# Optimization experiments

Hardware: AMD Instinct MI355X
Metric: run time of the kernel (lower is better)

The kernel has to match this reference:

```python
import jax, jax.numpy as jnp
import numpy as np

TAU, LBDA, THETA = 0.25, 0.15, 0.3
N_WARPS, N_ITERS = 5, 5
EPS = 1e-12  # GRAD_IS_ZERO


def centered_gradient(x):
    # centered [-0.5,0,0.5] stencil with one-sided boundaries (matches conv+boundary-fix)
    dx = jnp.concatenate([0.5 * (x[..., 1:2] - x[..., 0:1]),
                          0.5 * (x[..., 2:] - x[..., :-2]),
                          0.5 * (x[..., -1:] - x[..., -2:-1])], axis=-1)
    dy = jnp.concatenate([0.5 * (x[:, :, 1:2] - x[:, :, 0:1]),
                          0.5 * (x[:, :, 2:] - x[:, :, :-2]),
                          0.5 * (x[:, :, -1:] - x[:, :, -2:-1])], axis=2)
    return dx, dy


def forward_gradient(x):
    # [-1,1] forward difference, zero at last col/row (conv 'same' + zeroed last slice)
    dx = jnp.concatenate([x[..., 1:] - x[..., :-1], jnp.zeros_like(x[..., :1])], axis=-1)
    dy = jnp.concatenate([x[:, :, 1:] - x[:, :, :-1], jnp.zeros_like(x[:, :, :1])], axis=2)
    return dx, dy


def forward_divergence(px, py):
    # backward difference with zero left/top boundary; last entry = -p[-2]
    dx = jnp.concatenate([px[..., :1], px[..., 1:-1] - px[..., :-2], -px[..., -2:-1]], axis=-1)
    dy = jnp.concatenate([py[:, :, :1], py[:, :, 1:-1] - py[:, :, :-2], -py[:, :, -2:-1]], axis=2)
    return dx + dy


def warp_image(im, u, v):
    # bilinear warp by pixel flow (u,v); grid math mirrors the STN spatial_transformer:
    # normalized identity grid in [-1,1] plus flow*2/size, mapped back via (g+1)*size/2,
    # with indices clipped to the image (border behavior).
    B, C, H, W = im.shape
    dt = im.dtype
    gx = jnp.linspace(-1.0, 1.0, W, dtype=dt)[None, None, None, :]
    gy = jnp.linspace(-1.0, 1.0, H, dtype=dt)[None, None, :, None]
    x = (gx + u * (2.0 / W) + 1.0) * (W / 2.0)
    y = (gy + v * (2.0 / H) + 1.0) * (H / 2.0)
    x0 = jnp.floor(x).astype(jnp.int32)
    y0 = jnp.floor(y).astype(jnp.int32)
    x0i = jnp.clip(x0, 0, W - 1); x1i = jnp.clip(x0 + 1, 0, W - 1)
    y0i = jnp.clip(y0, 0, H - 1); y1i = jnp.clip(y0 + 1, 0, H - 1)
    x0f = x0i.astype(dt); x1f = x1i.astype(dt)
    y0f = y0i.astype(dt); y1f = y1i.astype(dt)
    flat = im.reshape(B, H * W)

    def gather(yi, xi):
        idx = (yi * W + xi).reshape(B, H * W)
        return jnp.take_along_axis(flat, idx, axis=1).reshape(B, C, H, W)

    Ia = gather(y0i, x0i); Ib = gather(y1i, x0i)
    Ic = gather(y0i, x1i); Id = gather(y1i, x1i)
    wa = (x1f - x) * (y1f - y); wb = (x1f - x) * (y - y0f)
    wc = (x - x0f) * (y1f - y); wd = (x - x0f) * (y - y0f)
    return wa * Ia + wb * Ib + wc * Ic + wd * Id


def tv_l1_scale(x1, x2, u1, u2):
    l_t = LBDA * THETA
    taut = TAU / THETA
    d2x, d2y = centered_gradient(x2)
    z = jnp.zeros_like(x1)
    p11, p12, p21, p22 = z, z, z, z
    rho = z
    for _ in range(N_WARPS):
        x2w = warp_image(x2, u1, u2)
        dxw = warp_image(d2x, u1, u2)
        dyw = warp_image(d2y, u1, u2)
        grad = dxw * dxw + dyw * dyw + EPS
        rho_c = x2w - dxw * u1 - dyw * u2 - x1
        for _ in range(N_ITERS):
            rho = rho_c + dxw * u1 + dyw * u2 + EPS
            m1 = rho < -l_t * grad
            m2 = rho > l_t * grad
            m3 = (~m1) & (~m2) & (grad > EPS)
            s = jnp.where(m1, l_t, jnp.where(m2, -l_t, jnp.where(m3, -rho / grad, 0.0)))
            v1 = s * dxw + u1
            v2 = s * dyw + u2
            u1 = v1 + THETA * forward_divergence(p11, p12)
            u2 = v2 + THETA * forward_divergence(p21, p22)
            u1x, u1y = forward_gradient(u1)
            u2x, u2y = forward_gradient(u2)
            n1 = 1.0 + taut * jnp.sqrt(u1x * u1x + u1y * u1y + EPS)
            n2 = 1.0 + taut * jnp.sqrt(u2x * u2x + u2y * u2y + EPS)
            p11 = (p11 + taut * u1x) / n1
            p12 = (p12 + taut * u1y) / n1
            p21 = (p21 + taut * u2x) / n2
            p22 = (p22 + taut * u2y) / n2
    return u1, u2, rho


def setup_inputs() -> dict:
    key = jax.random.key(0)
    k1, k2 = jax.random.split(key)
    B, H, W = 8, 480, 480
    x1 = jax.random.uniform(k1, (B, 1, H, W), dtype=jnp.float32)
    x2 = jax.random.uniform(k2, (B, 1, H, W), dtype=jnp.float32)
    u1 = jnp.zeros((B, 1, H, W), dtype=jnp.float32)
    u2 = jnp.zeros((B, 1, H, W), dtype=jnp.float32)
    return {"x1": x1, "x2": x2, "u1": u1, "u2": u2}


def reference(x1, x2, u1, u2):
    return tv_l1_scale(x1, x2, u1, u2)
```

## Files before the change

kernel.cpp:

```cpp
#include <hip/hip_runtime.h>

#pragma clang fp contract(off)


constexpr int B = 8, H = 480, W = 480;
constexpr int HW = H * W;
constexpr int N = B * HW;

constexpr float THETA = (float)0.3;
constexpr float L_T  = (float)(0.15 * 0.3);
constexpr float TAUT = (float)(0.25 / 0.3);
constexpr float EPSF = (float)1e-12;

#define RW 50
#define RH 40
#define HALO 5
#define TW (RW - 2*HALO)
#define TH (RH - 2*HALO)
#define NTX 12
#define NTY 16
#define TPB 512
#define NPX 4
#define RPX (RW*RH)

template <int LASTWARP>
__global__ __launch_bounds__(TPB, 4) void k_fused(
    const float* __restrict__ x1, const float* __restrict__ x2,
    const float* __restrict__ u1In, const float* __restrict__ u2In,
    const float* __restrict__ pIn,
    float* __restrict__ u1Out, float* __restrict__ u2Out,
    float* __restrict__ pOut,
    float* __restrict__ rhoOut)
{
  __shared__ float2 su[RH][RW];
  __shared__ float2 spA[RH][RW];
  __shared__ float2 spB[RH][RW];

  int blk = blockIdx.x;
  int bx = blk % NTX;
  int by = (blk / NTX) % NTY;
  int b  = blk / (NTX * NTY);
  int ox = bx * TW - HALO;
  int oy = by * TH - HALO;

  int tid = threadIdx.x;

  const float* __restrict__ im = x2 + b * HW;
  const int base = b * HW;

  float cdx[NPX], cdy[NPX], crc[NPX];

#pragma unroll
  for (int k = 0; k < NPX; ++k) {
    int idx = tid + k * TPB;
    if (idx < RPX) {
      int ly = idx / RW, lx = idx - ly * RW;
      int px = ox + lx, py = oy + ly;
      bool valid = (px >= 0 && px < W && py >= 0 && py < H);
      if (valid) {
        int gi = base + py * W + px;
        float u = u1In[gi], v = u2In[gi];
        const float step = 2.0f / 479.0f;
        float gx = -1.0f + (float)px * step;
        float gy = -1.0f + (float)py * step;
        float X = ((gx + u * (float)(2.0 / 480.0)) + 1.0f) * 240.0f;
        float Y = ((gy + v * (float)(2.0 / 480.0)) + 1.0f) * 240.0f;
        float fX = floorf(X), fY = floorf(Y);
        int ix = (int)fX, iy = (int)fY;
        int x0i = min(max(ix, 0), W - 1);
        int x1i = min(max(ix + 1, 0), W - 1);
        int y0i = min(max(iy, 0), H - 1);
        int y1i = min(max(iy + 1, 0), H - 1);
        float x0f = (float)x0i, x1f = (float)x1i;
        float y0f = (float)y0i, y1f = (float)y1i;
        float wa = (x1f - X) * (y1f - Y);
        float wb = (x1f - X) * (Y - y0f);
        float wc = (X - x0f) * (y1f - Y);
        float wd = (X - x0f) * (Y - y0f);
        auto at = [&](int yy, int xx) -> float { return im[yy * W + xx]; };
        auto dxc = [&](int yy, int xx) -> float {
          int xm = max(xx - 1, 0), xp = min(xx + 1, W - 1);
          return 0.5f * (at(yy, xp) - at(yy, xm));
        };
        auto dyc = [&](int yy, int xx) -> float {
          int ym = max(yy - 1, 0), yp = min(yy + 1, H - 1);
          return 0.5f * (at(yp, xx) - at(ym, xx));
        };
        float x2w = ((wa * at(y0i, x0i) + wb * at(y1i, x0i)) + wc * at(y0i, x1i)) + wd * at(y1i, x1i);
        float dxw = ((wa * dxc(y0i, x0i) + wb * dxc(y1i, x0i)) + wc * dxc(y0i, x1i)) + wd * dxc(y1i, x1i);
        float dyw = ((wa * dyc(y0i, x0i) + wb * dyc(y1i, x0i)) + wc * dyc(y0i, x1i)) + wd * dyc(y1i, x1i);
        cdx[k] = dxw; cdy[k] = dyw;
        crc[k] = ((x2w - dxw * u) - dyw * v) - x1[gi];
        float q11, q12, q21, q22;
        if (pIn) {
          q11 = pIn[0 * N + gi]; q12 = pIn[1 * N + gi];
          q21 = pIn[2 * N + gi]; q22 = pIn[3 * N + gi];
        } else { q11 = 0.f; q12 = 0.f; q21 = 0.f; q22 = 0.f; }
        su[ly][lx]  = make_float2(u, v);
        spA[ly][lx] = make_float2(q11, q21);
        spB[ly][lx] = make_float2(q12, q22);
      }
    }
  }
  __syncthreads();

  for (int t = 1; t <= 5; ++t) {
    int ulox = ox + t; if (ulox < 0) ulox = 0;
    int uloy = oy + t; if (uloy < 0) uloy = 0;
    int uhix = (ox + RW >= W) ? W : (ox + RW + 1 - t);
    int uhiy = (oy + RH >= H) ? H : (oy + RH + 1 - t);

#pragma unroll
    for (int k = 0; k < NPX; ++k) {
      int idx = tid + k * TPB;
      if (idx < RPX) {
        int ly = idx / RW, lx = idx - ly * RW;
        int px = ox + lx, py = oy + ly;
        if (px >= ulox && px < uhix && py >= uloy && py < uhiy) {
          float2 uo  = su[ly][lx];
          float2 pAo = spA[ly][lx];
          float2 pBo = spB[ly][lx];
          float2 pl = spA[ly][lx - 1];
          float2 pu = spB[ly - 1][lx];
          float dx = cdx[k], dy = cdy[k];
          float u = uo.x, v = uo.y;
          float rho = ((crc[k] + dx * u) + dy * v) + EPSF;
          float grad = (dx * dx + dy * dy) + EPSF;
          float lt_g = L_T * grad;
          float s;
          if (rho < -lt_g)      s = L_T;
          else if (rho > lt_g)  s = -L_T;
          else if (grad > EPSF) s = (-rho) / grad;
          else                  s = 0.f;
          float v1 = s * dx + u;
          float v2 = s * dy + v;
          float dvx1, dvy1, dvx2, dvy2;
          if (px == 0)          dvx1 = pAo.x;
          else if (px == W - 1) dvx1 = -pl.x;
          else                  dvx1 = pAo.x - pl.x;
          if (py == 0)          dvy1 = pBo.x;
          else if (py == H - 1) dvy1 = -pu.x;
          else                  dvy1 = pBo.x - pu.x;
          if (px == 0)          dvx2 = pAo.y;
          else if (px == W - 1) dvx2 = -pl.y;
          else                  dvx2 = pAo.y - pl.y;
          if (py == 0)          dvy2 = pBo.y;
          else if (py == H - 1) dvy2 = -pu.y;
          else                  dvy2 = pBo.y - pu.y;
          float nu1 = v1 + THETA * (dvx1 + dvy1);
          float nu2 = v2 + THETA * (dvx2 + dvy2);
          su[ly][lx] = make_float2(nu1, nu2);
          if (LASTWARP && t == 5) {
            int tx0 = bx * TW, ty0 = by * TH;
            if (px >= tx0 && px < tx0 + TW && py >= ty0 && py < ty0 + TH)
              rhoOut[base + py * W + px] = rho;
          }
        }
      }
    }
    __syncthreads();

    if (!(LASTWARP && t == 5)) {
      int phix = (ox + RW >= W) ? W : (ox + RW - t);
      int phiy = (oy + RH >= H) ? H : (oy + RH - t);
#pragma unroll
      for (int k = 0; k < NPX; ++k) {
        int idx = tid + k * TPB;
        if (idx < RPX) {
          int ly = idx / RW, lx = idx - ly * RW;
          int px = ox + lx, py = oy + ly;
          if (px >= ulox && px < phix && py >= uloy && py < phiy) {
            float2 uo = su[ly][lx];
            float2 uR = su[ly][lx + 1];
            float2 uD = su[ly + 1][lx];
            float2 pAo = spA[ly][lx];
            float2 pBo = spB[ly][lx];
            float u1c = uo.x, u2c = uo.y;
            float u1x = (px < W - 1) ? uR.x - u1c : 0.f;
            float u1y = (py < H - 1) ? uD.x - u1c : 0.f;
            float u2x = (px < W - 1) ? uR.y - u2c : 0.f;
            float u2y = (py < H - 1) ? uD.y - u2c : 0.f;
            float n1 = 1.0f + TAUT * sqrtf((u1x * u1x + u1y * u1y) + EPSF);
            float n2 = 1.0f + TAUT * sqrtf((u2x * u2x + u2y * u2y) + EPSF);
            float np11 = (pAo.x + TAUT * u1x) / n1;
            float np12 = (pBo.x + TAUT * u1y) / n1;
            float np21 = (pAo.y + TAUT * u2x) / n2;
            float np22 = (pBo.y + TAUT * u2y) / n2;
            spA[ly][lx] = make_float2(np11, np21);
            spB[ly][lx] = make_float2(np12, np22);
          }
        }
      }
    }
    __syncthreads();
  }

  int tx0 = bx * TW, ty0 = by * TH;
#pragma unroll
  for (int k = 0; k < NPX; ++k) {
    int idx = tid + k * TPB;
    if (idx < RPX) {
      int ly = idx / RW, lx = idx - ly * RW;
      int px = ox + lx, py = oy + ly;
      if (px >= tx0 && px < tx0 + TW && py >= ty0 && py < ty0 + TH) {
        int gi = base + py * W + px;
        float2 uo = su[ly][lx];
        u1Out[gi] = uo.x;
        u2Out[gi] = uo.y;
        if (!LASTWARP) {
          float2 pAo = spA[ly][lx];
          float2 pBo = spB[ly][lx];
          pOut[0 * N + gi] = pAo.x;
          pOut[1 * N + gi] = pBo.x;
          pOut[2 * N + gi] = pAo.y;
          pOut[3 * N + gi] = pBo.y;
        }
      }
    }
  }
}

extern "C" void kernel_launch(void* const* d_in, const int* in_sizes, int n_in,
                              void* d_out, int out_size, void* d_ws, size_t ws_size,
                              hipStream_t stream) {
  const float* x1 = (const float*)d_in[0];
  const float* x2 = (const float*)d_in[1];
  const float* u1_in = (const float*)d_in[2];
  const float* u2_in = (const float*)d_in[3];

  float* u1o  = (float*)d_out;
  float* u2o  = u1o + (size_t)N;
  float* rhoo = u1o + (size_t)2 * N;

  float* ws  = (float*)d_ws;
  float* uA1 = ws;
  float* uA2 = ws + (size_t)N;
  float* pA  = ws + (size_t)2 * N;
  float* uB1 = ws + (size_t)6 * N;
  float* uB2 = ws + (size_t)7 * N;
  float* pB  = ws + (size_t)8 * N;

  dim3 grd(NTX * NTY * B), blk(TPB);
  k_fused<0><<<grd, blk, 0, stream>>>(x1, x2, u1_in, u2_in, nullptr, uA1, uA2, pA, rhoo);
  k_fused<0><<<grd, blk, 0, stream>>>(x1, x2, uA1, uA2, pA, uB1, uB2, pB, rhoo);
  k_fused<0><<<grd, blk, 0, stream>>>(x1, x2, uB1, uB2, pB, uA1, uA2, pA, rhoo);
  k_fused<0><<<grd, blk, 0, stream>>>(x1, x2, uA1, uA2, pA, uB1, uB2, pB, rhoo);
  k_fused<1><<<grd, blk, 0, stream>>>(x1, x2, uB1, uB2, pB, u1o, u2o, pA, rhoo);
}
```

Before: 354.5 us.

## Interleave intermediate u/p state and specialize interior tiles without boundary checks

Intermediate flow and dual variables between warp launches are now stored interleaved, as float2 for u and float4 for p, so each pixel reads and writes state with one vector access instead of several strided scalar ones. Each block is dispatched to an interior or boundary template, and the interior version drops the image-edge clamps and divergence/gradient boundary branches. Local pixel coordinates are precomputed once per thread rather than recomputed with divisions every phase. The cost is roughly doubled code size from the two template instantiations, which may raise register pressure.

Result: slower. 365.9 us (+3.2%).

```diff
diff --git a/kernel.cpp b/kernel.cpp
--- a/kernel.cpp
+++ b/kernel.cpp
@@ -15,51 +15,53 @@
 #define RW 50
 #define RH 40
 #define HALO 5
-#define TW (RW - 2*HALO)
-#define TH (RH - 2*HALO)
+#define TW 40
+#define TH 30
 #define NTX 12
 #define NTY 16
 #define TPB 512
 #define NPX 4
 #define RPX (RW*RH)
 
-template <int LASTWARP>
-__global__ __launch_bounds__(TPB, 4) void k_fused(
+template <int WARPK, bool INTERIOR>
+__device__ __forceinline__ void run_body(
     const float* __restrict__ x1, const float* __restrict__ x2,
     const float* __restrict__ u1In, const float* __restrict__ u2In,
-    const float* __restrict__ pIn,
+    const float2* __restrict__ uIn, const float4* __restrict__ pIn,
     float* __restrict__ u1Out, float* __restrict__ u2Out,
-    float* __restrict__ pOut,
-    float* __restrict__ rhoOut)
+    float2* __restrict__ uOut, float4* __restrict__ pOut,
+    float* __restrict__ rhoOut,
+    int bx, int by, int b,
+    float2* __restrict__ su, float2* __restrict__ spA,
+    float2* __restrict__ spB)
 {
-  __shared__ float2 su[RH][RW];
-  __shared__ float2 spA[RH][RW];
-  __shared__ float2 spB[RH][RW];
-
-  int blk = blockIdx.x;
-  int bx = blk % NTX;
-  int by = (blk / NTX) % NTY;
-  int b  = blk / (NTX * NTY);
-  int ox = bx * TW - HALO;
-  int oy = by * TH - HALO;
-
-  int tid = threadIdx.x;
-
-  const float* __restrict__ im = x2 + b * HW;
+  const int ox = bx * TW - HALO;
+  const int oy = by * TH - HALO;
+  const int tid = threadIdx.x;
   const int base = b * HW;
+  const float* __restrict__ im = x2 + base;
 
   float cdx[NPX], cdy[NPX], crc[NPX];
+  int lxA[NPX], lyA[NPX];
+#pragma unroll
+  for (int k = 0; k < NPX; ++k) {
+    int idx = tid + k * TPB;
+    lyA[k] = idx / RW;
+    lxA[k] = idx - lyA[k] * RW;
+  }
 
 #pragma unroll
   for (int k = 0; k < NPX; ++k) {
     int idx = tid + k * TPB;
     if (idx < RPX) {
-      int ly = idx / RW, lx = idx - ly * RW;
+      int lx = lxA[k], ly = lyA[k];
       int px = ox + lx, py = oy + ly;
-      bool valid = (px >= 0 && px < W && py >= 0 && py < H);
+      bool valid = INTERIOR ? true : (px >= 0 && px < W && py >= 0 && py < H);
       if (valid) {
         int gi = base + py * W + px;
-        float u = u1In[gi], v = u2In[gi];
+        float u, v;
+        if (WARPK == 0) { u = u1In[gi]; v = u2In[gi]; }
+        else            { float2 uv = uIn[gi]; u = uv.x; v = uv.y; }
         const float step = 2.0f / 479.0f;
         float gx = -1.0f + (float)px * step;
         float gy = -1.0f + (float)py * step;
@@ -91,37 +93,41 @@
         float dyw = ((wa * dyc(y0i, x0i) + wb * dyc(y1i, x0i)) + wc * dyc(y0i, x1i)) + wd * dyc(y1i, x1i);
         cdx[k] = dxw; cdy[k] = dyw;
         crc[k] = ((x2w - dxw * u) - dyw * v) - x1[gi];
-        float q11, q12, q21, q22;
-        if (pIn) {
-          q11 = pIn[0 * N + gi]; q12 = pIn[1 * N + gi];
-          q21 = pIn[2 * N + gi]; q22 = pIn[3 * N + gi];
-        } else { q11 = 0.f; q12 = 0.f; q21 = 0.f; q22 = 0.f; }
-        su[ly][lx]  = make_float2(u, v);
-        spA[ly][lx] = make_float2(q11, q21);
-        spB[ly][lx] = make_float2(q12, q22);
+        float4 q;
+        if (WARPK == 0) q = make_float4(0.f, 0.f, 0.f, 0.f);
+        else            q = pIn[gi];
+        su[idx]  = make_float2(u, v);
+        spA[idx] = make_float2(q.x, q.z);
+        spB[idx] = make_float2(q.y, q.w);
       }
     }
   }
   __syncthreads();
 
   for (int t = 1; t <= 5; ++t) {
-    int ulox = ox + t; if (ulox < 0) ulox = 0;
-    int uloy = oy + t; if (uloy < 0) uloy = 0;
-    int uhix = (ox + RW >= W) ? W : (ox + RW + 1 - t);
-    int uhiy = (oy + RH >= H) ? H : (oy + RH + 1 - t);
+    int ulox, uloy, uhix, uhiy;
+    if (INTERIOR) {
+      ulox = ox + t; uloy = oy + t;
+      uhix = ox + RW + 1 - t; uhiy = oy + RH + 1 - t;
+    } else {
+      ulox = ox + t; if (ulox < 0) ulox = 0;
+      uloy = oy + t; if (uloy < 0) uloy = 0;
+      uhix = (ox + RW >= W) ? W : (ox + RW + 1 - t);
+      uhiy = (oy + RH >= H) ? H : (oy + RH + 1 - t);
+    }
 
 #pragma unroll
     for (int k = 0; k < NPX; ++k) {
       int idx = tid + k * TPB;
       if (idx < RPX) {
-        int ly = idx / RW, lx = idx - ly * RW;
+        int lx = lxA[k], ly = lyA[k];
         int px = ox + lx, py = oy + ly;
         if (px >= ulox && px < uhix && py >= uloy && py < uhiy) {
-          float2 uo  = su[ly][lx];
-          float2 pAo = spA[ly][lx];
-          float2 pBo = spB[ly][lx];
-          float2 pl = spA[ly][lx - 1];
-          float2 pu = spB[ly - 1][lx];
+          float2 uo  = su[idx];
+          float2 pAo = spA[idx];
+          float2 pBo = spB[idx];
+          float2 pl = spA[idx - 1];
+          float2 pu = spB[idx - RW];
           float dx = cdx[k], dy = cdy[k];
           float u = uo.x, v = uo.y;
           float rho = ((crc[k] + dx * u) + dy * v) + EPSF;
@@ -135,24 +141,30 @@
           float v1 = s * dx + u;
           float v2 = s * dy + v;
           float dvx1, dvy1, dvx2, dvy2;
-          if (px == 0)          dvx1 = pAo.x;
-          else if (px == W - 1) dvx1 = -pl.x;
-          else                  dvx1 = pAo.x - pl.x;
-          if (py == 0)          dvy1 = pBo.x;
-          else if (py == H - 1) dvy1 = -pu.x;
-          else                  dvy1 = pBo.x - pu.x;
-          if (px == 0)          dvx2 = pAo.y;
-          else if (px == W - 1) dvx2 = -pl.y;
-          else                  dvx2 = pAo.y - pl.y;
-          if (py == 0)          dvy2 = pBo.y;
-          else if (py == H - 1) dvy2 = -pu.y;
-          else                  dvy2 = pBo.y - pu.y;
+          if (INTERIOR) {
+            dvx1 = pAo.x - pl.x;
+            dvy1 = pBo.x - pu.x;
+            dvx2 = pAo.y - pl.y;
+            dvy2 = pBo.y - pu.y;
+          } else {
+            if (px == 0)          dvx1 = pAo.x;
+            else if (px == W - 1) dvx1 = -pl.x;
+            else                  dvx1 = pAo.x - pl.x;
+            if (py == 0)          dvy1 = pBo.x;
+            else if (py == H - 1) dvy1 = -pu.x;
+            else                  dvy1 = pBo.x - pu.x;
+            if (px == 0)          dvx2 = pAo.y;
+            else if (px == W - 1) dvx2 = -pl.y;
+            else                  dvx2 = pAo.y - pl.y;
+            if (py == 0)          dvy2 = pBo.y;
+            else if (py == H - 1) dvy2 = -pu.y;
+            else                  dvy2 = pBo.y - pu.y;
+          }
           float nu1 = v1 + THETA * (dvx1 + dvy1);
           float nu2 = v2 + THETA * (dvx2 + dvy2);
-          su[ly][lx] = make_float2(nu1, nu2);
-          if (LASTWARP && t == 5) {
-            int tx0 = bx * TW, ty0 = by * TH;
-            if (px >= tx0 && px < tx0 + TW && py >= ty0 && py < ty0 + TH)
+          su[idx] = make_float2(nu1, nu2);
+          if (WARPK == 2 && t == 5) {
+            if (lx >= HALO && lx < HALO + TW && ly >= HALO && ly < HALO + TH)
               rhoOut[base + py * W + px] = rho;
           }
         }
@@ -160,34 +172,44 @@
     }
     __syncthreads();
 
-    if (!(LASTWARP && t == 5)) {
-      int phix = (ox + RW >= W) ? W : (ox + RW - t);
-      int phiy = (oy + RH >= H) ? H : (oy + RH - t);
+    if (!(WARPK == 2 && t == 5)) {
+      int phix, phiy;
+      if (INTERIOR) { phix = ox + RW - t; phiy = oy + RH - t; }
+      else {
+        phix = (ox + RW >= W) ? W : (ox + RW - t);
+        phiy = (oy + RH >= H) ? H : (oy + RH - t);
+      }
 #pragma unroll
       for (int k = 0; k < NPX; ++k) {
         int idx = tid + k * TPB;
         if (idx < RPX) {
-          int ly = idx / RW, lx = idx - ly * RW;
+          int lx = lxA[k], ly = lyA[k];
           int px = ox + lx, py = oy + ly;
           if (px >= ulox && px < phix && py >= uloy && py < phiy) {
-            float2 uo = su[ly][lx];
-            float2 uR = su[ly][lx + 1];
-            float2 uD = su[ly + 1][lx];
-            float2 pAo = spA[ly][lx];
-            float2 pBo = spB[ly][lx];
+            float2 uo = su[idx];
+            float2 uR = su[idx + 1];
+            float2 uD = su[idx + RW];
+            float2 pAo = spA[idx];
+            float2 pBo = spB[idx];
             float u1c = uo.x, u2c = uo.y;
-            float u1x = (px < W - 1) ? uR.x - u1c : 0.f;
-            float u1y = (py < H - 1) ? uD.x - u1c : 0.f;
-            float u2x = (px < W - 1) ? uR.y - u2c : 0.f;
-            float u2y = (py < H - 1) ? uD.y - u2c : 0.f;
+            float u1x, u1y, u2x, u2y;
+            if (INTERIOR) {
+              u1x = uR.x - u1c; u1y = uD.x - u1c;
+              u2x = uR.y - u2c; u2y = uD.y - u2c;
+            } else {
+              u1x = (px < W - 1) ? uR.x - u1c : 0.f;
+              u1y = (py < H - 1) ? uD.x - u1c : 0.f;
+              u2x = (px < W - 1) ? uR.y - u2c : 0.f;
+              u2y = (py < H - 1) ? uD.y - u2c : 0.f;
+            }
             float n1 = 1.0f + TAUT * sqrtf((u1x * u1x + u1y * u1y) + EPSF);
             float n2 = 1.0f + TAUT * sqrtf((u2x * u2x + u2y * u2y) + EPSF);
             float np11 = (pAo.x + TAUT * u1x) / n1;
             float np12 = (pBo.x + TAUT * u1y) / n1;
             float np21 = (pAo.y + TAUT * u2x) / n2;
             float np22 = (pBo.y + TAUT * u2y) / n2;
-            spA[ly][lx] = make_float2(np11, np21);
-            spB[ly][lx] = make_float2(np12, np22);
+            spA[idx] = make_float2(np11, np21);
+            spB[idx] = make_float2(np12, np22);
           }
         }
       }
@@ -195,29 +217,48 @@
     __syncthreads();
   }
 
-  int tx0 = bx * TW, ty0 = by * TH;
 #pragma unroll
   for (int k = 0; k < NPX; ++k) {
     int idx = tid + k * TPB;
     if (idx < RPX) {
-      int ly = idx / RW, lx = idx - ly * RW;
-      int px = ox + lx, py = oy + ly;
-      if (px >= tx0 && px < tx0 + TW && py >= ty0 && py < ty0 + TH) {
-        int gi = base + py * W + px;
-        float2 uo = su[ly][lx];
-        u1Out[gi] = uo.x;
-        u2Out[gi] = uo.y;
-        if (!LASTWARP) {
-          float2 pAo = spA[ly][lx];
-          float2 pBo = spB[ly][lx];
-          pOut[0 * N + gi] = pAo.x;
-          pOut[1 * N + gi] = pBo.x;
-          pOut[2 * N + gi] = pAo.y;
-          pOut[3 * N + gi] = pBo.y;
+      int lx = lxA[k], ly = lyA[k];
+      if (lx >= HALO && lx < HALO + TW && ly >= HALO && ly < HALO + TH) {
+        int gi = base + (oy + ly) * W + (ox + lx);
+        float2 uo = su[idx];
+        if (WARPK == 2) {
+          u1Out[gi] = uo.x;
+          u2Out[gi] = uo.y;
+        } else {
+          uOut[gi] = uo;
+          float2 a = spA[idx], c = spB[idx];
+          pOut[gi] = make_float4(a.x, c.x, a.y, c.y);
         }
       }
     }
   }
+}
+
+template <int WARPK>
+__global__ __launch_bounds__(TPB, 4) void k_fused(
+    const float* __restrict__ x1, const float* __restrict__ x2,
+    const float* __restrict__ u1In, const float* __restrict__ u2In,
+    const float2* __restrict__ uIn, const float4* __restrict__ pIn,
+    float* __restrict__ u1Out, float* __restrict__ u2Out,
+    float2* __restrict__ uOut, float4* __restrict__ pOut,
+    float* __restrict__ rhoOut)
+{
+  __shared__ float2 su[RPX], spA[RPX], spB[RPX];
+  int blk = blockIdx.x;
+  int bx = blk % NTX;
+  int by = (blk / NTX) % NTY;
+  int b  = blk / (NTX * NTY);
+  bool interior = (bx > 0 && bx < NTX - 1 && by > 0 && by < NTY - 1);
+  if (interior)
+    run_body<WARPK, true >(x1, x2, u1In, u2In, uIn, pIn, u1Out, u2Out,
+                           uOut, pOut, rhoOut, bx, by, b, su, spA, spB);
+  else
+    run_body<WARPK, false>(x1, x2, u1In, u2In, uIn, pIn, u1Out, u2Out,
+                           uOut, pOut, rhoOut, bx, by, b, su, spA, spB);
 }
 
 extern "C" void kernel_launch(void* const* d_in, const int* in_sizes, int n_in,
@@ -233,17 +274,20 @@
   float* rhoo = u1o + (size_t)2 * N;
 
   float* ws  = (float*)d_ws;
-  float* uA1 = ws;
-  float* uA2 = ws + (size_t)N;
-  float* pA  = ws + (size_t)2 * N;
-  float* uB1 = ws + (size_t)6 * N;
-  float* uB2 = ws + (size_t)7 * N;
-  float* pB  = ws + (size_t)8 * N;
+  float2* uA = (float2*)ws;
+  float4* pA = (float4*)(ws + (size_t)2 * N);
+  float2* uB = (float2*)(ws + (size_t)6 * N);
+  float4* pB = (float4*)(ws + (size_t)8 * N);
 
   dim3 grd(NTX * NTY * B), blk(TPB);
-  k_fused<0><<<grd, blk, 0, stream>>>(x1, x2, u1_in, u2_in, nullptr, uA1, uA2, pA, rhoo);
-  k_fused<0><<<grd, blk, 0, stream>>>(x1, x2, uA1, uA2, pA, uB1, uB2, pB, rhoo);
-  k_fused<0><<<grd, blk, 0, stream>>>(x1, x2, uB1, uB2, pB, uA1, uA2, pA, rhoo);
-  k_fused<0><<<grd, blk, 0, stream>>>(x1, x2, uA1, uA2, pA, uB1, uB2, pB, rhoo);
-  k_fused<1><<<grd, blk, 0, stream>>>(x1, x2, uB1, uB2, pB, u1o, u2o, pA, rhoo);
+  k_fused<0><<<grd, blk, 0, stream>>>(x1, x2, u1_in, u2_in, nullptr, nullptr,
+                                      nullptr, nullptr, uA, pA, rhoo);
+  k_fused<1><<<grd, blk, 0, stream>>>(x1, x2, nullptr, nullptr, uA, pA,
+                                      nullptr, nullptr, uB, pB, rhoo);
+  k_fused<1><<<grd, blk, 0, stream>>>(x1, x2, nullptr, nullptr, uB, pB,
+                                      nullptr, nullptr, uA, pA, rhoo);
+  k_fused<1><<<grd, blk, 0, stream>>>(x1, x2, nullptr, nullptr, uA, pA,
+                                      nullptr, nullptr, uB, pB, rhoo);
+  k_fused<2><<<grd, blk, 0, stream>>>(x1, x2, nullptr, nullptr, uB, pB,
+                                      u1o, u2o, nullptr, nullptr, rhoo);
 }
```
